# Performance work log

Hardware: AMD Instinct MI355X
Metric: run time of the kernel (lower is better)

The kernel has to match this reference:

```python
import jax, jax.numpy as jnp
import numpy as np

BITS_I, BITS_W = 8, 8
GROUP = 36
DIR_I = (0, 1, 2, 3)
DIR_W = (0, 1, 2, 3)


def bfp_quantize(x, bits, group_size, perm):
    """Block floating point: groups of `group_size` elements (after permuting
    axes by `perm` and flattening) share one exponent (exponent of max abs);
    mantissas are rounded to `bits` signed bits."""
    inv_perm = tuple(np.argsort(perm))
    xp = jnp.transpose(x, perm)
    shape = xp.shape
    flat = xp.reshape(-1)
    n = flat.shape[0]
    pad = (-n) % group_size
    flat = jnp.pad(flat, (0, pad))
    g = flat.reshape(-1, group_size)
    maxabs = jnp.max(jnp.abs(g), axis=1, keepdims=True)
    e = jnp.floor(jnp.log2(jnp.maximum(maxabs, jnp.float32(1e-38))))
    scale = jnp.exp2(e - (bits - 1))  # shared group exponent, `bits` mantissa bits
    qmax = 2 ** (bits - 1) - 1
    q = jnp.clip(jnp.round(g / scale), -qmax - 1, qmax) * scale
    q = jnp.where(maxabs == 0, jnp.float32(0), q)
    out = q.reshape(-1)[:n].reshape(shape)
    return jnp.transpose(out, inv_perm)


def conv2d(x, w, b, stride=1, padding=1, dilation=1, groups=1):
    out = jax.lax.conv_general_dilated(
        x, w,
        window_strides=(stride, stride),
        padding=[(padding, padding), (padding, padding)],
        rhs_dilation=(dilation, dilation),
        feature_group_count=groups,
        dimension_numbers=('NCHW', 'OIHW', 'NCHW'))
    if b is not None:
        out = out + b[None, :, None, None]
    return out


def setup_inputs() -> dict:
    key = jax.random.key(0)
    k1, k2, k3 = jax.random.split(key, 3)
    x = jax.random.normal(k1, (16, 256, 56, 56), dtype=jnp.float32)
    fan_in = 256 * 3 * 3
    bound = 1.0 / np.sqrt(fan_in)
    weight = jax.random.uniform(k2, (256, 256, 3, 3), dtype=jnp.float32,
                                minval=-np.sqrt(6.0 / fan_in), maxval=np.sqrt(6.0 / fan_in))
    bias = jax.random.uniform(k3, (256,), dtype=jnp.float32, minval=-bound, maxval=bound)
    return {"x": x, "weight": weight, "bias": bias}


def reference(x, weight, bias):
    xq = bfp_quantize(x, BITS_I, GROUP, DIR_I)
    wq = bfp_quantize(weight, BITS_W, GROUP, DIR_W)
    return conv2d(xq, wq, bias, stride=1, padding=1, dilation=1, groups=1)
```

## Files before the change

### kernel.cpp

```cpp
#include <hip/hip_runtime.h>

typedef short short8 __attribute__((ext_vector_type(8)));
typedef float f32x4 __attribute__((ext_vector_type(4)));
typedef unsigned short u16;
typedef __attribute__((address_space(3))) unsigned lds_u32_t;
typedef __attribute__((address_space(1))) const unsigned glb_u32_t;

namespace {
constexpr int NIMG = 16;
constexpr int CIN  = 256;
constexpr int HIMG = 56;
constexpr int WIMG = 56;
constexpr int KOUT = 256;
constexpr int PIX  = HIMG * WIMG;
constexpr int HPAD = 58;
constexpr int PP   = HPAD * HPAD;
constexpr int TILES = 26;
constexpr int NX   = NIMG * CIN * PIX;
constexpr int NWEL = KOUT * CIN * 9;
constexpr int XQ_HALVES = NIMG * 32 * PP * 8;
constexpr int MAXB = XQ_HALVES - 8;
constexpr int CHUNK = 8 * PIX;
constexpr int XBLK = NIMG * 32;
constexpr int WB   = 64;
}

__global__ __launch_bounds__(256) void quant_fused(
        const float* __restrict__ x, u16* __restrict__ xq2,
        const float* __restrict__ wsrc, u16* __restrict__ wt3) {
    __shared__ u16 ot[CHUNK];
    const int b = blockIdx.x;
    const int t = threadIdx.x;

    if (b < XBLK) {
        const long s  = (long)b * CHUNK;
        const int  g0 = (int)(s / 36);
        const int  g1 = (int)((s + CHUNK - 1) / 36);

        if (t < 228) {
            int ph, pw;
            if (t < 58)       { ph = 0;  pw = t; }
            else if (t < 116) { ph = 57; pw = t - 58; }
            else { int r = t - 116; ph = 1 + (r >> 1); pw = (r & 1) * 57; }
            *(uint4*)(xq2 + ((size_t)b * PP + ph * HPAD + pw) * 8) =
                make_uint4(0, 0, 0, 0);
        }

        for (int g = g0 + t; g <= g1; g += 256) {
            const long e0 = (long)g * 36;
            float v[36];
            if (e0 + 36 <= (long)NX) {
                const float4* p4 = (const float4*)(x + e0);
#pragma unroll
                for (int j = 0; j < 9; j++) {
                    float4 q4 = p4[j];
                    v[4*j+0] = q4.x; v[4*j+1] = q4.y;
                    v[4*j+2] = q4.z; v[4*j+3] = q4.w;
                }
            } else {
                for (int j = 0; j < 36; j++)
                    v[j] = (e0 + j < (long)NX) ? x[e0 + j] : 0.f;
            }
            float ma = 0.f;
#pragma unroll
            for (int j = 0; j < 36; j++) ma = fmaxf(ma, fabsf(v[j]));
            float scale = 0.f, rinv = 0.f;
            if (ma != 0.f) {
                float e = floorf(log2f(ma));
                scale = exp2f(e - 7.f);
                rinv  = exp2f(7.f - e);
            }
            const long o = e0 - s;
#pragma unroll
            for (int j = 0; j < 36; j += 2) {
                float qa = fminf(fmaxf(rintf(v[j]   * rinv), -128.f), 127.f) * scale;
                float qb = fminf(fmaxf(rintf(v[j+1] * rinv), -128.f), 127.f) * scale;
                uint pk = (__float_as_uint(qa) >> 16)
                        | ((__float_as_uint(qb) >> 16) << 16);
                long oo = o + j;
                if (oo >= 0 && oo < CHUNK)
                    *(uint*)&ot[oo] = pk;
            }
        }
        __syncthreads();

        for (int p = t; p < PIX; p += 256) {
            short8 o8;
#pragma unroll
            for (int cl = 0; cl < 8; cl++)
                o8[cl] = (short)ot[cl * PIX + p];
            int ph = p / WIMG + 1, pw = p % WIMG + 1;
            *(short8*)(xq2 + ((size_t)b * PP + ph * HPAD + pw) * 8) = o8;
        }
    } else {
        int g = (b - XBLK) * 256 + t;
        int base = g * 36;
        float v[36];
        const float4* p4 = (const float4*)(wsrc + base);
#pragma unroll
        for (int j = 0; j < 9; j++) {
            float4 tt = p4[j];
            v[4*j+0] = tt.x; v[4*j+1] = tt.y; v[4*j+2] = tt.z; v[4*j+3] = tt.w;
        }
        float ma = 0.f;
#pragma unroll
        for (int j = 0; j < 36; j++) ma = fmaxf(ma, fabsf(v[j]));
        float scale = 0.f, rinv = 0.f;
        if (ma != 0.f) {
            float e = floorf(log2f(ma));
            scale = exp2f(e - 7.f);
            rinv  = exp2f(7.f - e);
        }
        int k  = g >> 6;
        int c0 = (g & 63) * 4;
#pragma unroll
        for (int j = 0; j < 36; j++) {
            float q = rintf(v[j] * rinv);
            q = fminf(fmaxf(q, -128.f), 127.f) * scale;
            int c  = c0 + j / 9;
            int rs = j % 9;
            int idx = ((((rs * 4 + (c >> 6)) * 8 + ((c >> 3) & 7)) * KOUT) + k) * 8 + (c & 7);
            wt3[idx] = (u16)(__float_as_uint(q) >> 16);
        }
    }
}

#define ISSUE(csp_, rs_, buf_)                                                 \
    {                                                                          \
        const int xoff8_ = (((rs_) / 3) * HPAD + ((rs_) % 3)) * 8;             \
        const int sA_ = ((rs_) * 4 + (csp_)) * 16384;                          \
        const int sB_ = (csp_) * 8 * PP * 8;                                   \
        _Pragma("unroll")                                                      \
        for (int kl = 0; kl < 2; kl++) {                                       \
            _Pragma("unroll")                                                  \
            for (int hl = 0; hl < 2; hl++) {                                   \
                __builtin_amdgcn_global_load_lds(                              \
                    (glb_u32_t*)(wt3 + sA_ + kl * 2048 + hl * 512 + aL),       \
                    (lds_u32_t*)(lA[buf_] + wv * 2048 + kl * 1024 + hl * 512   \
                                 + lane * 8),                                  \
                    16, 0, 0);                                                 \
                int bi = bB + sB_ + kl * (PP * 8) + xoff8_ + hl * 512;         \
                bi = min(bi, MAXB);           \
                __builtin_amdgcn_global_load_lds(                              \
                    (glb_u32_t*)(xq2 + bi),                                    \
                    (lds_u32_t*)(lB[buf_] + wv * 2048 + kl * 1024 + hl * 512   \
                                 + lane * 8),                                  \
                    16, 0, 0);                                                 \
            }                                                                  \
        }                                                                      \
    }

__global__ __launch_bounds__(256) void conv_kernel(
        const u16* __restrict__ xq2, const u16* __restrict__ wt3,
        const float* __restrict__ bias, float* __restrict__ out) {
    __shared__ u16 lA[2][8192];
    __shared__ u16 lB[2][8192];

    const int tid  = threadIdx.x;
    const int lane = tid & 63;
    const int wv   = tid >> 6;
    const int bx   = blockIdx.x;
    const int n    = bx / TILES;
    const int t0   = (bx % TILES) * 128;
    const int k0   = blockIdx.y * 128;

    const int aL = (k0 + lane) * 8 + wv * 4096;
    const int bB = ((n * 32 + 2 * wv) * PP + t0 + lane) * 8;

    const int frow = lane & 15;
    const int fkk  = lane >> 4;
    const int fAo = (fkk * 128 + (wv >> 1) * 64 + frow) * 8;
    const int fBo = (fkk * 128 + (wv & 1) * 64 + frow) * 8;

    f32x4 acc[4][4] = {};

    ISSUE(0, 0, 0);

#pragma unroll
    for (int st = 0; st < 36; st++) {
        const int buf = st & 1;
        if (st < 35) {
            ISSUE((st + 1) / 9, (st + 1) % 9, (st + 1) & 1);
            asm volatile("s_waitcnt vmcnt(8)" ::: "memory");
        } else {
            asm volatile("s_waitcnt vmcnt(0)" ::: "memory");
        }
        __builtin_amdgcn_s_barrier();
        __builtin_amdgcn_sched_barrier(0);

#pragma unroll
        for (int ks = 0; ks < 2; ks++) {
            short8 af[4], bf[4];
#pragma unroll
            for (int i = 0; i < 4; i++)
                af[i] = *(const short8*)(lA[buf] + ks * 4096 + fAo + i * 128);
#pragma unroll
            for (int j = 0; j < 4; j++)
                bf[j] = *(const short8*)(lB[buf] + ks * 4096 + fBo + j * 128);
#pragma unroll
            for (int i = 0; i < 4; i++)
#pragma unroll
                for (int j = 0; j < 4; j++)
                    acc[i][j] = __builtin_amdgcn_mfma_f32_16x16x32_bf16(
                        af[i], bf[j], acc[i][j], 0, 0, 0);
        }

        __builtin_amdgcn_sched_barrier(0);
        __builtin_amdgcn_s_barrier();
    }

    const int kbase = k0 + (wv >> 1) * 64 + fkk * 4;
    const int mbase = (wv & 1) * 64 + frow;
#pragma unroll
    for (int j = 0; j < 4; j++) {
        int ppp = t0 + mbase + j * 16;
        int h = ppp / HPAD, w = ppp % HPAD;
        if (w < WIMG && h < HIMG) {
            float* ob = out + (size_t)n * KOUT * PIX + h * WIMG + w;
#pragma unroll
            for (int i = 0; i < 4; i++) {
                int kch = kbase + i * 16;
#pragma unroll
                for (int r = 0; r < 4; r++)
                    ob[(size_t)(kch + r) * PIX] = acc[i][j][r] + bias[kch + r];
            }
        }
    }
}

extern "C" void kernel_launch(void* const* d_in, const int* in_sizes, int n_in,
                              void* d_out, int out_size, void* d_ws, size_t ws_size,
                              hipStream_t stream) {
    const float* x   = (const float*)d_in[0];
    const float* wgt = (const float*)d_in[1];
    const float* bs  = (const float*)d_in[2];
    float* out = (float*)d_out;

    u16* xq2 = (u16*)d_ws;
    u16* wt3 = xq2 + XQ_HALVES;

    quant_fused<<<XBLK + WB, 256, 0, stream>>>(x, xq2, wgt, wt3);
    conv_kernel<<<dim3(NIMG * TILES, 2), 256, 0, stream>>>(xq2, wt3, bs, out);
}
```

Measured before the change: 183.9 us.

## Switch conv main loop to triple-buffered half-stages with single barrier

```diff
diff --git a/kernel.cpp b/kernel.cpp
--- a/kernel.cpp
+++ b/kernel.cpp
@@ -125,36 +125,31 @@
     }
 }
 
-#define ISSUE(csp_, rs_, buf_)                                                 \
+#define ISSUE3(csp_, rs_, sub_, qb_)                                           \
     {                                                                          \
         const int xoff8_ = (((rs_) / 3) * HPAD + ((rs_) % 3)) * 8;             \
-        const int sA_ = ((rs_) * 4 + (csp_)) * 16384;                          \
-        const int sB_ = (csp_) * 8 * PP * 8;                                   \
+        const int sA_ = ((rs_) * 4 + (csp_)) * 16384 + (sub_) * 8192;          \
+        const int sB_ = ((csp_) * 8 + (sub_) * 4) * PP * 8;                    \
         _Pragma("unroll")                                                      \
-        for (int kl = 0; kl < 2; kl++) {                                       \
-            _Pragma("unroll")                                                  \
-            for (int hl = 0; hl < 2; hl++) {                                   \
-                __builtin_amdgcn_global_load_lds(                              \
-                    (glb_u32_t*)(wt3 + sA_ + kl * 2048 + hl * 512 + aL),       \
-                    (lds_u32_t*)(lA[buf_] + wv * 2048 + kl * 1024 + hl * 512   \
-                                 + lane * 8),                                  \
-                    16, 0, 0);                                                 \
-                int bi = bB + sB_ + kl * (PP * 8) + xoff8_ + hl * 512;         \
-                bi = min(bi, MAXB);           \
-                __builtin_amdgcn_global_load_lds(                              \
-                    (glb_u32_t*)(xq2 + bi),                                    \
-                    (lds_u32_t*)(lB[buf_] + wv * 2048 + kl * 1024 + hl * 512   \
-                                 + lane * 8),                                  \
-                    16, 0, 0);                                                 \
-            }                                                                  \
+        for (int hl = 0; hl < 2; hl++) {                                       \
+            __builtin_amdgcn_global_load_lds(                                  \
+                (glb_u32_t*)(wt3 + sA_ + hl * 512 + aLw),                      \
+                (lds_u32_t*)(lA3[qb_] + hl * 512 + dstw),                      \
+                16, 0, 0);                                                     \
+            int bi_ = bBw + sB_ + xoff8_ + hl * 512;                           \
+            bi_ = min(bi_, MAXB);       \
+            __builtin_amdgcn_global_load_lds(                                  \
+                (glb_u32_t*)(xq2 + bi_),                                       \
+                (lds_u32_t*)(lB3[qb_] + hl * 512 + dstw),                      \
+                16, 0, 0);                                                     \
         }                                                                      \
     }
 
 __global__ __launch_bounds__(256) void conv_kernel(
         const u16* __restrict__ xq2, const u16* __restrict__ wt3,
         const float* __restrict__ bias, float* __restrict__ out) {
-    __shared__ u16 lA[2][8192];
-    __shared__ u16 lB[2][8192];
+    __shared__ u16 lA3[3][4096];
+    __shared__ u16 lB3[3][4096];
 
     const int tid  = threadIdx.x;
     const int lane = tid & 63;
@@ -164,8 +159,9 @@
     const int t0   = (bx % TILES) * 128;
     const int k0   = blockIdx.y * 128;
 
-    const int aL = (k0 + lane) * 8 + wv * 4096;
-    const int bB = ((n * 32 + 2 * wv) * PP + t0 + lane) * 8;
+    const int aLw  = (k0 + lane) * 8 + wv * 2048;
+    const int bBw  = ((n * 32 + wv) * PP + t0 + lane) * 8;
+    const int dstw = wv * 1024 + lane * 8;
 
     const int frow = lane & 15;
     const int fkk  = lane >> 4;
@@ -174,39 +170,39 @@
 
     f32x4 acc[4][4] = {};
 
-    ISSUE(0, 0, 0);
-
-#pragma unroll
-    for (int st = 0; st < 36; st++) {
-        const int buf = st & 1;
-        if (st < 35) {
-            ISSUE((st + 1) / 9, (st + 1) % 9, (st + 1) & 1);
-            asm volatile("s_waitcnt vmcnt(8)" ::: "memory");
-        } else {
-            asm volatile("s_waitcnt vmcnt(0)" ::: "memory");
-        }
+    ISSUE3(0, 0, 0, 0);
+    ISSUE3(0, 0, 1, 1);
+
+#pragma unroll
+    for (int h = 0; h < 72; h++) {
+        if (h < 71) asm volatile("s_waitcnt vmcnt(4)" ::: "memory");
+        else        asm volatile("s_waitcnt vmcnt(0)" ::: "memory");
         __builtin_amdgcn_s_barrier();
         __builtin_amdgcn_sched_barrier(0);
 
-#pragma unroll
-        for (int ks = 0; ks < 2; ks++) {
-            short8 af[4], bf[4];
-#pragma unroll
-            for (int i = 0; i < 4; i++)
-                af[i] = *(const short8*)(lA[buf] + ks * 4096 + fAo + i * 128);
+        const int hb = h % 3;
+        short8 af[4], bf[4];
+#pragma unroll
+        for (int i = 0; i < 4; i++)
+            af[i] = *(const short8*)(lA3[hb] + fAo + i * 128);
+#pragma unroll
+        for (int j = 0; j < 4; j++)
+            bf[j] = *(const short8*)(lB3[hb] + fBo + j * 128);
+
+        __builtin_amdgcn_s_setprio(1);
+#pragma unroll
+        for (int i = 0; i < 4; i++)
 #pragma unroll
             for (int j = 0; j < 4; j++)
-                bf[j] = *(const short8*)(lB[buf] + ks * 4096 + fBo + j * 128);
-#pragma unroll
-            for (int i = 0; i < 4; i++)
-#pragma unroll
-                for (int j = 0; j < 4; j++)
-                    acc[i][j] = __builtin_amdgcn_mfma_f32_16x16x32_bf16(
-                        af[i], bf[j], acc[i][j], 0, 0, 0);
-        }
-
+                acc[i][j] = __builtin_amdgcn_mfma_f32_16x16x32_bf16(
+                    af[i], bf[j], acc[i][j], 0, 0, 0);
+        __builtin_amdgcn_s_setprio(0);
         __builtin_amdgcn_sched_barrier(0);
-        __builtin_amdgcn_s_barrier();
+
+        if (h + 2 < 72) {
+            const int h2 = h + 2;
+            ISSUE3(h2 / 18, (h2 / 2) % 9, h2 & 1, h2 % 3);
+        }
     }
 
     const int kbase = k0 + (wv >> 1) * 64 + fkk * 4;
```

Result: no change. 186.8 us (+1.6%).
